# Kernel optimization log

Hardware: AMD Instinct MI355X
Metric: run time of the kernel (lower is better)

Reference implementation:

```python
import jax, jax.numpy as jnp
import numpy as np

B, CIN, COUT, H, W, K = 4, 128, 128, 128, 128, 3
KK = K * K


def setup_inputs() -> dict:
    key = jax.random.key(0)
    ks = jax.random.split(key, 6)
    return {
        "inp": jax.random.normal(ks[0], (B, CIN, H, W), jnp.float32),
        "feat": jax.random.normal(ks[1], (B, CIN, H, W), jnp.float32),
        # small offset-conv weights keep predicted offsets in a realistic few-pixel range
        "w_off": jax.random.normal(ks[2], (3 * KK, CIN, K, K), jnp.float32) * 0.01,
        "b_off": jnp.zeros((3 * KK,), jnp.float32),
        "w_dc": jax.random.normal(ks[3], (COUT, CIN, K, K), jnp.float32) * (1.0 / np.sqrt(CIN * KK)),
        "b_dc": jnp.zeros((COUT,), jnp.float32),
    }


def _conv3x3(x, w, b):
    # stride=1, padding=1, dilation=1, groups=1 (module defaults)
    y = jax.lax.conv_general_dilated(x, w, (1, 1), ((1, 1), (1, 1)),
                                     dimension_numbers=("NCHW", "OIHW", "NCHW"))
    return y + b[None, :, None, None]


def _modulated_deform_conv(x, offset, mask, w, b):
    # DCNv2: offset [B, 2*KK, H, W] interleaved (y, x) per kernel tap, mask [B, KK, H, W]
    b_, c, h, wd = x.shape
    ky = jnp.repeat(jnp.arange(K), K)  # kernel row index per tap, [KK]
    kx = jnp.tile(jnp.arange(K), K)    # kernel col index per tap, [KK]
    off = offset.reshape(b_, KK, 2, h, wd)
    # sampling positions: out_idx - pad + k*dilation + learned offset
    py = off[:, :, 0] + (jnp.arange(h)[None, None, :, None] + ky[None, :, None, None] - 1).astype(offset.dtype)
    px = off[:, :, 1] + (jnp.arange(wd)[None, None, None, :] + kx[None, :, None, None] - 1).astype(offset.dtype)
    y0 = jnp.floor(py)
    x0 = jnp.floor(px)
    ly = py - y0  # bilinear fractions (grad flows to offsets through these)
    lx = px - x0
    y0i = y0.astype(jnp.int32)
    x0i = x0.astype(jnp.int32)
    x_flat = x.reshape(b_, c, h * wd)

    def corner(yi, xi, wgt):
        valid = (yi >= 0) & (yi < h) & (xi >= 0) & (xi < wd)  # zero padding outside
        idx = jnp.clip(yi, 0, h - 1) * wd + jnp.clip(xi, 0, wd - 1)
        g = jnp.take_along_axis(x_flat, idx.reshape(b_, 1, -1), axis=2).reshape(b_, c, KK, h, wd)
        return g * (wgt * valid)[:, None]

    val = (corner(y0i,     x0i,     (1 - ly) * (1 - lx))
         + corner(y0i,     x0i + 1, (1 - ly) * lx)
         + corner(y0i + 1, x0i,     ly * (1 - lx))
         + corner(y0i + 1, x0i + 1, ly * lx))
    val = val * mask[:, None]  # modulation
    out = jnp.einsum("bckhw,ock->bohw", val, w.reshape(w.shape[0], c, KK))
    return out + b[None, :, None, None]


def reference(inp, feat, w_off, b_off, w_dc, b_dc):
    o = _conv3x3(feat, w_off, b_off)
    o1, o2, m = jnp.split(o, 3, axis=1)
    offset = jnp.concatenate([o1, o2], axis=1)
    mask = jax.nn.sigmoid(m)
    return _modulated_deform_conv(inp, offset, mask, w_dc, b_dc)
```

## Files before the change

### kernel.cpp

```cpp
#include <hip/hip_runtime.h>
#include <math.h>

#define B_    4
#define CIN_  128
#define COUT_ 128
#define H_    128
#define W_    128
#define HW_   (H_*W_)
#define KK_   9

typedef __attribute__((ext_vector_type(8))) short short8;
typedef __attribute__((ext_vector_type(4))) float f32x4;
typedef _Float16 h8 __attribute__((ext_vector_type(8)));
typedef float f2v __attribute__((ext_vector_type(2), aligned(4)));

static __device__ __forceinline__ unsigned f2bf(float f) {
    union { float f; unsigned u; } v; v.f = f;
    return (v.u + 0x7fffu + ((v.u >> 16) & 1u)) >> 16;
}
static __device__ __forceinline__ unsigned short f2h(float f) {
    union { _Float16 h; unsigned short u; } v; v.h = (_Float16)f;
    return v.u;
}


__global__ __launch_bounds__(256) void tpose_kernel(
    const float* __restrict__ inp, unsigned short* __restrict__ inpT)
{
    const int by = blockIdx.x;
    const int b = by >> 7, y = by & 127;
    __shared__ unsigned short s_T[128 * 142];

    const float* src = inp + (size_t)b * CIN_ * HW_ + y * W_;
    const int xs = (threadIdx.x & 63) * 2;
    const int c0 = threadIdx.x >> 6;
#pragma unroll 4
    for (int p = 0; p < 32; ++p) {
        int c = c0 + 4 * p;
        f2v d = *(const f2v*)(src + (size_t)c * HW_ + xs);
        s_T[xs * 142 + c]       = f2h(d.x);
        s_T[(xs + 1) * 142 + c] = f2h(d.y);
    }
    __syncthreads();

    unsigned short* dst = inpT + (size_t)by * (W_ * CIN_);
    const int cs = (threadIdx.x & 15) * 8;
    const int x0 = threadIdx.x >> 4;
#pragma unroll
    for (int p = 0; p < 8; ++p) {
        int x = x0 + 16 * p;
        unsigned r[4];
#pragma unroll
        for (int j = 0; j < 4; ++j) {
            unsigned lo = s_T[x * 142 + cs + 2 * j];
            unsigned hi = s_T[x * 142 + cs + 2 * j + 1];
            r[j] = lo | (hi << 16);
        }
        *(int4*)(dst + (size_t)x * CIN_ + cs) = make_int4(r[0], r[1], r[2], r[3]);
    }
}

__global__ __launch_bounds__(256) void wswz_kernel(
    const float* __restrict__ w_dc, unsigned short* __restrict__ w_swz)
{
    int idx = blockIdx.x * 256 + threadIdx.x;
    int q   = idx >> 9;
    int rem = idx & 511;
    int ocb = rem >> 6;
    int l   = rem & 63;
    int cbq = q / 9;
    int k   = q - cbq * 9;
    int cb  = (cbq << 5) + ((l >> 4) << 3);
    int oc  = (ocb << 4) + (l & 15);
    unsigned r[4];
#pragma unroll
    for (int j = 0; j < 4; ++j) {
        float f0 = w_dc[((size_t)(oc * CIN_ + cb + 2 * j    )) * KK_ + k];
        float f1 = w_dc[((size_t)(oc * CIN_ + cb + 2 * j + 1)) * KK_ + k];
        r[j] = (unsigned)f2h(f0) | ((unsigned)f2h(f1) << 16);
    }
    *(int4*)&w_swz[(size_t)idx * 8] = make_int4(r[0], r[1], r[2], r[3]);
}

__global__ __launch_bounds__(256) void woffswz_kernel(
    const float* __restrict__ w_off, unsigned short* __restrict__ woff_swz)
{
    int idx = blockIdx.x * 256 + threadIdx.x;
    int q   = idx >> 7;
    int rem = idx & 127;
    int l   = rem & 63;
    int cbq = q / 9;
    int k   = q - cbq * 9;
    int cb  = (cbq << 5) + ((l >> 4) << 3);
    int oc  = ((rem >> 6) << 4) + (l & 15);
    unsigned r[4];
#pragma unroll
    for (int j = 0; j < 4; ++j) {
        float f0 = 0.f, f1 = 0.f;
        if (oc < 27) {
            f0 = w_off[((size_t)(oc * CIN_ + cb + 2 * j    )) * KK_ + k];
            f1 = w_off[((size_t)(oc * CIN_ + cb + 2 * j + 1)) * KK_ + k];
        }
        r[j] = f2bf(f0) | (f2bf(f1) << 16);
    }
    *(int4*)&woff_swz[(size_t)idx * 8] = make_int4(r[0], r[1], r[2], r[3]);
}

__global__ __launch_bounds__(256, 4) void offset_mfma_kernel(
    const float* __restrict__ feat, const unsigned short* __restrict__ woff_swz,
    const float* __restrict__ b_off, float* __restrict__ offm)
{
    const int tid = threadIdx.x;
    const int bx = blockIdx.x;
    const int lidx = ((bx & 7) << 7) | (bx >> 3);
    const int b  = lidx >> 8;
    const int h  = (lidx & 255) >> 1;
    const int w0 = (lidx & 1) << 6;

    __shared__ unsigned short s_F[3][66][40];

    const int lane = tid & 63;
    const int wave = tid >> 6;
    const int kg = lane >> 4, pn = lane & 15;

    const float* fbase = feat + (size_t)b * CIN_ * HW_;

    f32x4 acc[2];
    acc[0] = (f32x4){0.f, 0.f, 0.f, 0.f};
    acc[1] = (f32x4){0.f, 0.f, 0.f, 0.f};

    for (int cb = 0; cb < 4; ++cb) {
        if (cb) __syncthreads();

#pragma unroll
        for (int r = 0; r < 3; ++r) {
            const int y = h + r - 1;
            const bool yv = (unsigned)y < (unsigned)H_;
            const float* rowp = fbase + (size_t)(cb << 5) * HW_ + y * W_;
#pragma unroll
            for (int j = 0; j < 4; ++j) {
                int item = tid + (j << 8);
                int c = item >> 5;
                int e = item & 31;
                int x0 = w0 - 1 + 2 * e;
                int hx = min(max(x0, 0), W_ - 2);
                float v0 = 0.f, v1 = 0.f;
                if (yv) {
                    f2v p = *(const f2v*)(rowp + (size_t)c * HW_ + hx);
                    v0 = (x0 == hx) ? p.x : ((x0 < hx) ? 0.f : p.y);
                    v1 = (x0 == hx) ? p.y : ((x0 < hx) ? p.x : 0.f);
                }
                s_F[r][2 * e    ][c] = (unsigned short)f2bf(v0);
                s_F[r][2 * e + 1][c] = (unsigned short)f2bf(v1);
            }
            if (tid < 32) {
                int c = tid;
                int x0 = w0 + 63;
                int hx = min(x0, W_ - 2);
                float v0 = 0.f, v1 = 0.f;
                if (yv) {
                    f2v p = *(const f2v*)(rowp + (size_t)c * HW_ + hx);
                    v0 = (x0 == hx) ? p.x : p.y;
                    v1 = (x0 == hx) ? p.y : 0.f;
                }
                s_F[r][64][c] = (unsigned short)f2bf(v0);
                s_F[r][65][c] = (unsigned short)f2bf(v1);
            }
        }
        __syncthreads();

        const int qb2 = cb * 18;
        const short8* wb = (const short8*)woff_swz;
        short8 a0 = wb[(size_t)(qb2    ) * 64 + lane];
        short8 a1 = wb[(size_t)(qb2 + 1) * 64 + lane];
#pragma unroll
        for (int k = 0; k < 9; ++k) {
            const int ky = k / 3, kx = k - 3 * ky;
            short8 bfr = *(const short8*)&s_F[ky][wave * 16 + pn + kx][kg * 8];
            short8 na0, na1;
            if (k < 8) {
                na0 = wb[(size_t)(qb2 + 2 * k + 2) * 64 + lane];
                na1 = wb[(size_t)(qb2 + 2 * k + 3) * 64 + lane];
            }
            acc[0] = __builtin_amdgcn_mfma_f32_16x16x32_bf16(a0, bfr, acc[0], 0, 0, 0);
            acc[1] = __builtin_amdgcn_mfma_f32_16x16x32_bf16(a1, bfr, acc[1], 0, 0, 0);
            if (k < 8) { a0 = na0; a1 = na1; }
        }
    }

    const int row0 = (lane >> 4) << 2;
    const int col  = lane & 15;
    const int pw   = w0 + wave * 16 + col;
#pragma unroll
    for (int mt = 0; mt < 2; ++mt) {
#pragma unroll
        for (int i = 0; i < 4; ++i) {
            int oc = mt * 16 + row0 + i;
            if (oc < 27) {
                float v = acc[mt][i] + b_off[oc];
                if (oc >= 18) v = 1.f / (1.f + __expf(-v));
                offm[((size_t)(b * 27 + oc)) * HW_ + h * W_ + pw] = v;
            }
        }
    }
}

__global__ __launch_bounds__(256, 4) void dcn_mfma_kernel(
    const unsigned short* __restrict__ inpT, const float* __restrict__ offm,
    const unsigned short* __restrict__ w_swz, const float* __restrict__ b_dc,
    float* __restrict__ out)
{
    const int tid = threadIdx.x;
    const int bx = blockIdx.x;
    const int lidx = ((bx & 7) << 7) | (bx >> 3);
    const int b   = lidx >> 8;
    const int h   = (lidx & 255) >> 1;
    const int pw0 = (lidx & 1) << 6;

    __shared__ int2   s_midx[576];
    __shared__ float4 s_mwgt[576];
    __shared__ unsigned short s_V[2][64][40];

    for (int i = tid; i < 576; i += 256) {
        int k = i >> 6, p = i & 63;
        int ky = k / 3, kx = k - ky * 3;
        int pw = pw0 + p;
        const float* ob = offm + (size_t)b * 27 * HW_ + h * W_ + pw;
        float offy = ob[(2 * k    ) * HW_];
        float offx = ob[(2 * k + 1) * HW_];
        float mask = ob[(18 + k   ) * HW_];
        float py = offy + (float)(h  + ky - 1);
        float px_ = offx + (float)(pw + kx - 1);
        float y0f = floorf(py), x0f = floorf(px_);
        float ly = py - y0f, lx = px_ - x0f;
        int y0 = (int)y0f, x0 = (int)x0f;
        int y1 = y0 + 1;
        int hx = min(max(x0, 0), W_ - 2);
        float wlo = 0.f, whi = 0.f;
        if (x0 == hx)          { wlo = 1.f - lx; whi = lx; }
        else if (x0 == hx - 1) { wlo = lx; }
        else if (x0 == hx + 1) { whi = 1.f - lx; }
        float wt_top = ((unsigned)y0 < (unsigned)H_) ? (1.f - ly) * mask : 0.f;
        float wt_bot = ((unsigned)y1 < (unsigned)H_) ? ly * mask : 0.f;
        int cy0 = min(max(y0, 0), H_ - 1), cy1 = min(max(y1, 0), H_ - 1);
        s_midx[i] = make_int2(cy0 * W_ + hx, cy1 * W_ + hx);
        s_mwgt[i] = make_float4(wt_top * wlo, wt_top * whi,
                                wt_bot * wlo, wt_bot * whi);
    }

    const int lane = tid & 63;
    const int wave = tid >> 6;
    const int kg = lane >> 4, pn = lane & 15;
    const int px = tid >> 2;
    const int cs = tid & 3;

    const char* inpTb = (const char*)(inpT + (size_t)b * CIN_ * HW_);

    f32x4 acc[2][4];
#pragma unroll
    for (int mt = 0; mt < 2; ++mt)
#pragma unroll
        for (int nt = 0; nt < 4; ++nt) acc[mt][nt] = (f32x4){0.f, 0.f, 0.f, 0.f};

    h8 pf0, pf1, pf2, pf3;

    auto issue = [&](int qq) {
        int cbq = qq / 9;
        int k   = qq - cbq * 9;
        int2 id = s_midx[(k << 6) + px];
        int coff = (cbq << 6) + (cs << 4);
        const char* g0 = inpTb + ((size_t)(unsigned)id.x << 8) + coff;
        const char* g1 = inpTb + ((size_t)(unsigned)id.y << 8) + coff;
        pf0 = *(const h8*)(g0);
        pf1 = *(const h8*)(g0 + 256);
        pf2 = *(const h8*)(g1);
        pf3 = *(const h8*)(g1 + 256);
    };

    __syncthreads();
    issue(0);

    for (int q = 0; q < 36; ++q) {
        int k = q - (q / 9) * 9;

        float4 wt = s_mwgt[(k << 6) + px];
        h8 v = pf0 * (_Float16)wt.x;
        v += pf1 * (_Float16)wt.y;
        v += pf2 * (_Float16)wt.z;
        v += pf3 * (_Float16)wt.w;

        const h8* wp = (const h8*)w_swz + (size_t)(q * 8 + wave * 2) * 64 + lane;
        h8 af0 = wp[0];
        h8 af1 = wp[64];

        *(h8*)&s_V[q & 1][px][cs << 3] = v;

        int qn = (q + 1 < 36) ? q + 1 : 35;
        issue(qn);

        __syncthreads();

#pragma unroll
        for (int nt = 0; nt < 4; ++nt) {
            h8 bfr = *(const h8*)&s_V[q & 1][nt * 16 + pn][kg * 8];
            acc[0][nt] = __builtin_amdgcn_mfma_f32_16x16x32_f16(af0, bfr, acc[0][nt], 0, 0, 0);
            acc[1][nt] = __builtin_amdgcn_mfma_f32_16x16x32_f16(af1, bfr, acc[1][nt], 0, 0, 0);
        }
    }

    const int row0 = (lane >> 4) << 2;
    const int col  = lane & 15;
#pragma unroll
    for (int mt = 0; mt < 2; ++mt) {
#pragma unroll
        for (int nt = 0; nt < 4; ++nt) {
            int pw = pw0 + nt * 16 + col;
#pragma unroll
            for (int i = 0; i < 4; ++i) {
                int oc = wave * 32 + mt * 16 + row0 + i;
                out[((size_t)(b * COUT_ + oc)) * HW_ + h * W_ + pw] =
                    acc[mt][nt][i] + b_dc[oc];
            }
        }
    }
}

extern "C" void kernel_launch(void* const* d_in, const int* in_sizes, int n_in,
                              void* d_out, int out_size, void* d_ws, size_t ws_size,
                              hipStream_t stream)
{
    const float* inp   = (const float*)d_in[0];
    const float* feat  = (const float*)d_in[1];
    const float* w_off = (const float*)d_in[2];
    const float* b_off = (const float*)d_in[3];
    const float* w_dc  = (const float*)d_in[4];
    const float* b_dc  = (const float*)d_in[5];
    float* out  = (float*)d_out;
    float* offm = (float*)d_ws;
    unsigned short* w_swz    = (unsigned short*)((char*)d_ws + 7077888);
    unsigned short* woff_swz = (unsigned short*)((char*)d_ws + 7077888 + 294912);
    unsigned short* inpT     = (unsigned short*)((char*)d_ws + 7446528);

    tpose_kernel<<<dim3(512), dim3(256), 0, stream>>>(inp, inpT);
    woffswz_kernel<<<dim3(18), dim3(256), 0, stream>>>(w_off, woff_swz);
    wswz_kernel<<<dim3(72), dim3(256), 0, stream>>>(w_dc, w_swz);
    offset_mfma_kernel<<<dim3(1024), dim3(256), 0, stream>>>(feat, woff_swz, b_off, offm);
    dcn_mfma_kernel<<<dim3(1024), dim3(256), 0, stream>>>(inpT, offm, w_swz, b_dc, out);
}
```

Before: 186.7 us.

## Fuse offset conv into deformable conv kernel and merge prep kernels

The three preprocessing kernels (input transpose, weight swizzles) are merged into one launch dispatched by block index. The offset/mask convolution is fused into the deformable-conv kernel, so offsets stay in shared memory instead of passing through a global workspace buffer. Shared memory is aliased between the feature tile and the sampled-value buffer. The per-thread pixel/channel mapping for the gather also changes from px=tid>>2 to px=tid&63, which alters the gather's memory access pattern. This removes two launches and the offset-map round trip, at the cost of a longer single kernel with more shared memory and possibly fewer resident blocks.

```diff
diff --git a/kernel.cpp b/kernel.cpp
--- a/kernel.cpp
+++ b/kernel.cpp
@@ -24,91 +24,89 @@
 }
 
 
-__global__ __launch_bounds__(256) void tpose_kernel(
-    const float* __restrict__ inp, unsigned short* __restrict__ inpT)
+__global__ __launch_bounds__(256) void prep_kernel(
+    const float* __restrict__ inp, const float* __restrict__ w_dc,
+    const float* __restrict__ w_off, unsigned short* __restrict__ inpT,
+    unsigned short* __restrict__ w_swz, unsigned short* __restrict__ woff_swz)
 {
-    const int by = blockIdx.x;
-    const int b = by >> 7, y = by & 127;
+    const int bx = blockIdx.x;
+    const int tid = threadIdx.x;
     __shared__ unsigned short s_T[128 * 142];
 
-    const float* src = inp + (size_t)b * CIN_ * HW_ + y * W_;
-    const int xs = (threadIdx.x & 63) * 2;
-    const int c0 = threadIdx.x >> 6;
+    if (bx < 512) {
+        const int b = bx >> 7, y = bx & 127;
+        const float* src = inp + (size_t)b * CIN_ * HW_ + y * W_;
+        const int xs = (tid & 63) * 2;
+        const int c0 = tid >> 6;
 #pragma unroll 4
-    for (int p = 0; p < 32; ++p) {
-        int c = c0 + 4 * p;
-        f2v d = *(const f2v*)(src + (size_t)c * HW_ + xs);
-        s_T[xs * 142 + c]       = f2h(d.x);
-        s_T[(xs + 1) * 142 + c] = f2h(d.y);
-    }
-    __syncthreads();
-
-    unsigned short* dst = inpT + (size_t)by * (W_ * CIN_);
-    const int cs = (threadIdx.x & 15) * 8;
-    const int x0 = threadIdx.x >> 4;
-#pragma unroll
-    for (int p = 0; p < 8; ++p) {
-        int x = x0 + 16 * p;
+        for (int p = 0; p < 32; ++p) {
+            int c = c0 + 4 * p;
+            f2v d = *(const f2v*)(src + (size_t)c * HW_ + xs);
+            s_T[xs * 142 + c]       = f2h(d.x);
+            s_T[(xs + 1) * 142 + c] = f2h(d.y);
+        }
+        __syncthreads();
+        unsigned short* dst = inpT + (size_t)bx * (W_ * CIN_);
+        const int cs = (tid & 15) * 8;
+        const int x0 = tid >> 4;
+#pragma unroll
+        for (int p = 0; p < 8; ++p) {
+            int x = x0 + 16 * p;
+            unsigned r[4];
+#pragma unroll
+            for (int j = 0; j < 4; ++j) {
+                unsigned lo = s_T[x * 142 + cs + 2 * j];
+                unsigned hi = s_T[x * 142 + cs + 2 * j + 1];
+                r[j] = lo | (hi << 16);
+            }
+            *(int4*)(dst + (size_t)x * CIN_ + cs) = make_int4(r[0], r[1], r[2], r[3]);
+        }
+    } else if (bx < 584) {
+        int idx = (bx - 512) * 256 + tid;
+        int q   = idx >> 9;
+        int rem = idx & 511;
+        int ocb = rem >> 6;
+        int l   = rem & 63;
+        int cbq = q / 9;
+        int k   = q - cbq * 9;
+        int cb  = (cbq << 5) + ((l >> 4) << 3);
+        int oc  = (ocb << 4) + (l & 15);
         unsigned r[4];
 #pragma unroll
         for (int j = 0; j < 4; ++j) {
-            unsigned lo = s_T[x * 142 + cs + 2 * j];
-            unsigned hi = s_T[x * 142 + cs + 2 * j + 1];
-            r[j] = lo | (hi << 16);
-        }
-        *(int4*)(dst + (size_t)x * CIN_ + cs) = make_int4(r[0], r[1], r[2], r[3]);
-    }
-}
-
-__global__ __launch_bounds__(256) void wswz_kernel(
-    const float* __restrict__ w_dc, unsigned short* __restrict__ w_swz)
-{
-    int idx = blockIdx.x * 256 + threadIdx.x;
-    int q   = idx >> 9;
-    int rem = idx & 511;
-    int ocb = rem >> 6;
-    int l   = rem & 63;
-    int cbq = q / 9;
-    int k   = q - cbq * 9;
-    int cb  = (cbq << 5) + ((l >> 4) << 3);
-    int oc  = (ocb << 4) + (l & 15);
-    unsigned r[4];
-#pragma unroll
-    for (int j = 0; j < 4; ++j) {
-        float f0 = w_dc[((size_t)(oc * CIN_ + cb + 2 * j    )) * KK_ + k];
-        float f1 = w_dc[((size_t)(oc * CIN_ + cb + 2 * j + 1)) * KK_ + k];
-        r[j] = (unsigned)f2h(f0) | ((unsigned)f2h(f1) << 16);
-    }
-    *(int4*)&w_swz[(size_t)idx * 8] = make_int4(r[0], r[1], r[2], r[3]);
-}
-
-__global__ __launch_bounds__(256) void woffswz_kernel(
-    const float* __restrict__ w_off, unsigned short* __restrict__ woff_swz)
-{
-    int idx = blockIdx.x * 256 + threadIdx.x;
-    int q   = idx >> 7;
-    int rem = idx & 127;
-    int l   = rem & 63;
-    int cbq = q / 9;
-    int k   = q - cbq * 9;
-    int cb  = (cbq << 5) + ((l >> 4) << 3);
-    int oc  = ((rem >> 6) << 4) + (l & 15);
-    unsigned r[4];
-#pragma unroll
-    for (int j = 0; j < 4; ++j) {
-        float f0 = 0.f, f1 = 0.f;
-        if (oc < 27) {
-            f0 = w_off[((size_t)(oc * CIN_ + cb + 2 * j    )) * KK_ + k];
-            f1 = w_off[((size_t)(oc * CIN_ + cb + 2 * j + 1)) * KK_ + k];
-        }
-        r[j] = f2bf(f0) | (f2bf(f1) << 16);
-    }
-    *(int4*)&woff_swz[(size_t)idx * 8] = make_int4(r[0], r[1], r[2], r[3]);
-}
-
-__global__ __launch_bounds__(256, 4) void offset_mfma_kernel(
-    const float* __restrict__ feat, const unsigned short* __restrict__ woff_swz,
-    const float* __restrict__ b_off, float* __restrict__ offm)
+            float f0 = w_dc[((size_t)(oc * CIN_ + cb + 2 * j    )) * KK_ + k];
+            float f1 = w_dc[((size_t)(oc * CIN_ + cb + 2 * j + 1)) * KK_ + k];
+            r[j] = (unsigned)f2h(f0) | ((unsigned)f2h(f1) << 16);
+        }
+        *(int4*)&w_swz[(size_t)idx * 8] = make_int4(r[0], r[1], r[2], r[3]);
+    } else {
+        int idx = (bx - 584) * 256 + tid;
+        int q   = idx >> 7;
+        int rem = idx & 127;
+        int l   = rem & 63;
+        int cbq = q / 9;
+        int k   = q - cbq * 9;
+        int cb  = (cbq << 5) + ((l >> 4) << 3);
+        int oc  = ((rem >> 6) << 4) + (l & 15);
+        unsigned r[4];
+#pragma unroll
+        for (int j = 0; j < 4; ++j) {
+            float f0 = 0.f, f1 = 0.f;
+            if (oc < 27) {
+                f0 = w_off[((size_t)(oc * CIN_ + cb + 2 * j    )) * KK_ + k];
+                f1 = w_off[((size_t)(oc * CIN_ + cb + 2 * j + 1)) * KK_ + k];
+            }
+            r[j] = f2bf(f0) | (f2bf(f1) << 16);
+        }
+        *(int4*)&woff_swz[(size_t)idx * 8] = make_int4(r[0], r[1], r[2], r[3]);
+    }
+}
+
+__global__ __launch_bounds__(256, 4) void fused_kernel(
+    const float* __restrict__ feat, const unsigned short* __restrict__ inpT,
+    const unsigned short* __restrict__ woff_swz, const unsigned short* __restrict__ w_swz,
+    const float* __restrict__ b_off, const float* __restrict__ b_dc,
+    float* __restrict__ out)
 {
     const int tid = threadIdx.x;
     const int bx = blockIdx.x;
@@ -117,119 +115,108 @@
     const int h  = (lidx & 255) >> 1;
     const int w0 = (lidx & 1) << 6;
 
-    __shared__ unsigned short s_F[3][66][40];
+    __shared__ __align__(16) char smem[36736];
+    unsigned short (*s_F)[66][40] = (unsigned short (*)[66][40])smem;
+    unsigned short *s_Vb          = (unsigned short*)smem;
+    float  (*offv)[65]            = (float (*)[65])(smem + 15872);
+    int2   *s_midx                = (int2  *)(smem + 15872 + 7040);
+    float4 *s_mwgt                = (float4*)(smem + 15872 + 7040 + 4608);
 
     const int lane = tid & 63;
     const int wave = tid >> 6;
     const int kg = lane >> 4, pn = lane & 15;
 
-    const float* fbase = feat + (size_t)b * CIN_ * HW_;
-
-    f32x4 acc[2];
-    acc[0] = (f32x4){0.f, 0.f, 0.f, 0.f};
-    acc[1] = (f32x4){0.f, 0.f, 0.f, 0.f};
-
-    for (int cb = 0; cb < 4; ++cb) {
-        if (cb) __syncthreads();
-
-#pragma unroll
-        for (int r = 0; r < 3; ++r) {
-            const int y = h + r - 1;
-            const bool yv = (unsigned)y < (unsigned)H_;
-            const float* rowp = fbase + (size_t)(cb << 5) * HW_ + y * W_;
-#pragma unroll
-            for (int j = 0; j < 4; ++j) {
-                int item = tid + (j << 8);
-                int c = item >> 5;
-                int e = item & 31;
-                int x0 = w0 - 1 + 2 * e;
-                int hx = min(max(x0, 0), W_ - 2);
-                float v0 = 0.f, v1 = 0.f;
-                if (yv) {
-                    f2v p = *(const f2v*)(rowp + (size_t)c * HW_ + hx);
-                    v0 = (x0 == hx) ? p.x : ((x0 < hx) ? 0.f : p.y);
-                    v1 = (x0 == hx) ? p.y : ((x0 < hx) ? p.x : 0.f);
+    {
+        const float* fbase = feat + (size_t)b * CIN_ * HW_;
+        f32x4 acc[2];
+        acc[0] = (f32x4){0.f, 0.f, 0.f, 0.f};
+        acc[1] = (f32x4){0.f, 0.f, 0.f, 0.f};
+
+        for (int cb = 0; cb < 4; ++cb) {
+            if (cb) __syncthreads();
+
+#pragma unroll
+            for (int r = 0; r < 3; ++r) {
+                const int y = h + r - 1;
+                const bool yv = (unsigned)y < (unsigned)H_;
+                const float* rowp = fbase + (size_t)(cb << 5) * HW_ + y * W_;
+#pragma unroll
+                for (int j = 0; j < 4; ++j) {
+                    int item = tid + (j << 8);
+                    int c = item >> 5;
+                    int e = item & 31;
+                    int x0 = w0 - 1 + 2 * e;
+                    int hx = min(max(x0, 0), W_ - 2);
+                    float v0 = 0.f, v1 = 0.f;
+                    if (yv) {
+                        f2v p = *(const f2v*)(rowp + (size_t)c * HW_ + hx);
+                        v0 = (x0 == hx) ? p.x : ((x0 < hx) ? 0.f : p.y);
+                        v1 = (x0 == hx) ? p.y : ((x0 < hx) ? p.x : 0.f);
+                    }
+                    s_F[r][2 * e    ][c] = (unsigned short)f2bf(v0);
+                    s_F[r][2 * e + 1][c] = (unsigned short)f2bf(v1);
                 }
-                s_F[r][2 * e    ][c] = (unsigned short)f2bf(v0);
-                s_F[r][2 * e + 1][c] = (unsigned short)f2bf(v1);
-            }
-            if (tid < 32) {
-                int c = tid;
-                int x0 = w0 + 63;
-                int hx = min(x0, W_ - 2);
-                float v0 = 0.f, v1 = 0.f;
-                if (yv) {
-                    f2v p = *(const f2v*)(rowp + (size_t)c * HW_ + hx);
-                    v0 = (x0 == hx) ? p.x : p.y;
-                    v1 = (x0 == hx) ? p.y : 0.f;
+                if (tid < 32) {
+                    int c = tid;
+                    int x0 = w0 + 63;
+                    int hx = min(x0, W_ - 2);
+                    float v0 = 0.f, v1 = 0.f;
+                    if (yv) {
+                        f2v p = *(const f2v*)(rowp + (size_t)c * HW_ + hx);
+                        v0 = (x0 == hx) ? p.x : p.y;
+                        v1 = (x0 == hx) ? p.y : 0.f;
+                    }
+                    s_F[r][64][c] = (unsigned short)f2bf(v0);
+                    s_F[r][65][c] = (unsigned short)f2bf(v1);
                 }
-                s_F[r][64][c] = (unsigned short)f2bf(v0);
-                s_F[r][65][c] = (unsigned short)f2bf(v1);
-            }
-        }
-        __syncthreads();
-
-        const int qb2 = cb * 18;
-        const short8* wb = (const short8*)woff_swz;
-        short8 a0 = wb[(size_t)(qb2    ) * 64 + lane];
-        short8 a1 = wb[(size_t)(qb2 + 1) * 64 + lane];
-#pragma unroll
-        for (int k = 0; k < 9; ++k) {
-            const int ky = k / 3, kx = k - 3 * ky;
-            short8 bfr = *(const short8*)&s_F[ky][wave * 16 + pn + kx][kg * 8];
-            short8 na0, na1;
-            if (k < 8) {
-                na0 = wb[(size_t)(qb2 + 2 * k + 2) * 64 + lane];
-                na1 = wb[(size_t)(qb2 + 2 * k + 3) * 64 + lane];
-            }
-            acc[0] = __builtin_amdgcn_mfma_f32_16x16x32_bf16(a0, bfr, acc[0], 0, 0, 0);
-            acc[1] = __builtin_amdgcn_mfma_f32_16x16x32_bf16(a1, bfr, acc[1], 0, 0, 0);
-            if (k < 8) { a0 = na0; a1 = na1; }
-        }
-    }
-
-    const int row0 = (lane >> 4) << 2;
-    const int col  = lane & 15;
-    const int pw   = w0 + wave * 16 + col;
-#pragma unroll
-    for (int mt = 0; mt < 2; ++mt) {
-#pragma unroll
-        for (int i = 0; i < 4; ++i) {
-            int oc = mt * 16 + row0 + i;
-            if (oc < 27) {
-                float v = acc[mt][i] + b_off[oc];
-                if (oc >= 18) v = 1.f / (1.f + __expf(-v));
-                offm[((size_t)(b * 27 + oc)) * HW_ + h * W_ + pw] = v;
-            }
-        }
-    }
-}
-
-__global__ __launch_bounds__(256, 4) void dcn_mfma_kernel(
-    const unsigned short* __restrict__ inpT, const float* __restrict__ offm,
-    const unsigned short* __restrict__ w_swz, const float* __restrict__ b_dc,
-    float* __restrict__ out)
-{
-    const int tid = threadIdx.x;
-    const int bx = blockIdx.x;
-    const int lidx = ((bx & 7) << 7) | (bx >> 3);
-    const int b   = lidx >> 8;
-    const int h   = (lidx & 255) >> 1;
-    const int pw0 = (lidx & 1) << 6;
-
-    __shared__ int2   s_midx[576];
-    __shared__ float4 s_mwgt[576];
-    __shared__ unsigned short s_V[2][64][40];
+            }
+            __syncthreads();
+
+            const int qb2 = cb * 18;
+            const short8* wb = (const short8*)woff_swz;
+            short8 a0 = wb[(size_t)(qb2    ) * 64 + lane];
+            short8 a1 = wb[(size_t)(qb2 + 1) * 64 + lane];
+#pragma unroll
+            for (int k = 0; k < 9; ++k) {
+                const int ky = k / 3, kx = k - 3 * ky;
+                short8 bfr = *(const short8*)&s_F[ky][wave * 16 + pn + kx][kg * 8];
+                short8 na0, na1;
+                if (k < 8) {
+                    na0 = wb[(size_t)(qb2 + 2 * k + 2) * 64 + lane];
+                    na1 = wb[(size_t)(qb2 + 2 * k + 3) * 64 + lane];
+                }
+                acc[0] = __builtin_amdgcn_mfma_f32_16x16x32_bf16(a0, bfr, acc[0], 0, 0, 0);
+                acc[1] = __builtin_amdgcn_mfma_f32_16x16x32_bf16(a1, bfr, acc[1], 0, 0, 0);
+                if (k < 8) { a0 = na0; a1 = na1; }
+            }
+        }
+
+        const int row0 = (lane >> 4) << 2;
+        const int col  = lane & 15;
+        const int pwl  = wave * 16 + col;
+#pragma unroll
+        for (int mt = 0; mt < 2; ++mt) {
+#pragma unroll
+            for (int i = 0; i < 4; ++i) {
+                int oc = mt * 16 + row0 + i;
+                if (oc < 27) {
+                    float v = acc[mt][i] + b_off[oc];
+                    if (oc >= 18) v = 1.f / (1.f + __expf(-v));
+                    offv[oc][pwl] = v;
+                }
+            }
+        }
+    }
+    __syncthreads();
 
     for (int i = tid; i < 576; i += 256) {
         int k = i >> 6, p = i & 63;
         int ky = k / 3, kx = k - ky * 3;
-        int pw = pw0 + p;
-        const float* ob = offm + (size_t)b * 27 * HW_ + h * W_ + pw;
-        float offy = ob[(2 * k    ) * HW_];
-        float offx = ob[(2 * k + 1) * HW_];
-        float mask = ob[(18 + k   ) * HW_];
-        float py = offy + (float)(h  + ky - 1);
+        int pw = w0 + p;
+        float offy = offv[2 * k    ][p];
+        float offx = offv[2 * k + 1][p];
+        float mask = offv[18 + k   ][p];
+        float py  = offy + (float)(h  + ky - 1);
         float px_ = offx + (float)(pw + kx - 1);
         float y0f = floorf(py), x0f = floorf(px_);
         float ly = py - y0f, lx = px_ - x0f;
@@ -247,20 +234,17 @@
         s_mwgt[i] = make_float4(wt_top * wlo, wt_top * whi,
                                 wt_bot * wlo, wt_bot * whi);
     }
-
-    const int lane = tid & 63;
-    const int wave = tid >> 6;
-    const int kg = lane >> 4, pn = lane & 15;
-    const int px = tid >> 2;
-    const int cs = tid & 3;
-
+    __syncthreads();
+
+    const int px = tid & 63;
+    const int cs = tid >> 6;
     const char* inpTb = (const char*)(inpT + (size_t)b * CIN_ * HW_);
 
-    f32x4 acc[2][4];
+    f32x4 acc2[2][4];
 #pragma unroll
     for (int mt = 0; mt < 2; ++mt)
 #pragma unroll
-        for (int nt = 0; nt < 4; ++nt) acc[mt][nt] = (f32x4){0.f, 0.f, 0.f, 0.f};
+        for (int nt = 0; nt < 4; ++nt) acc2[mt][nt] = (f32x4){0.f, 0.f, 0.f, 0.f};
 
     h8 pf0, pf1, pf2, pf3;
 
@@ -277,7 +261,6 @@
         pf3 = *(const h8*)(g1 + 256);
     };
 
-    __syncthreads();
     issue(0);
 
     for (int q = 0; q < 36; ++q) {
@@ -293,7 +276,7 @@
         h8 af0 = wp[0];
         h8 af1 = wp[64];
 
-        *(h8*)&s_V[q & 1][px][cs << 3] = v;
+        *(h8*)&s_Vb[(size_t)(q & 1) * (64 * 40) + px * 40 + (cs << 3)] = v;
 
         int qn = (q + 1 < 36) ? q + 1 : 35;
         issue(qn);
@@ -302,9 +285,9 @@
 
 #pragma unroll
         for (int nt = 0; nt < 4; ++nt) {
-            h8 bfr = *(const h8*)&s_V[q & 1][nt * 16 + pn][kg * 8];
-            acc[0][nt] = __builtin_amdgcn_mfma_f32_16x16x32_f16(af0, bfr, acc[0][nt], 0, 0, 0);
-            acc[1][nt] = __builtin_amdgcn_mfma_f32_16x16x32_f16(af1, bfr, acc[1][nt], 0, 0, 0);
+            h8 bfr = *(const h8*)&s_Vb[(size_t)(q & 1) * (64 * 40) + (nt * 16 + pn) * 40 + kg * 8];
+            acc2[0][nt] = __builtin_amdgcn_mfma_f32_16x16x32_f16(af0, bfr, acc2[0][nt], 0, 0, 0);
+            acc2[1][nt] = __builtin_amdgcn_mfma_f32_16x16x32_f16(af1, bfr, acc2[1][nt], 0, 0, 0);
         }
     }
 
@@ -314,12 +297,12 @@
     for (int mt = 0; mt < 2; ++mt) {
 #pragma unroll
         for (int nt = 0; nt < 4; ++nt) {
-            int pw = pw0 + nt * 16 + col;
+            int pw = w0 + nt * 16 + col;
 #pragma unroll
             for (int i = 0; i < 4; ++i) {
                 int oc = wave * 32 + mt * 16 + row0 + i;
                 out[((size_t)(b * COUT_ + oc)) * HW_ + h * W_ + pw] =
-                    acc[mt][nt][i] + b_dc[oc];
+                    acc2[mt][nt][i] + b_dc[oc];
             }
         }
     }
@@ -336,14 +319,10 @@
     const float* w_dc  = (const float*)d_in[4];
     const float* b_dc  = (const float*)d_in[5];
     float* out  = (float*)d_out;
-    float* offm = (float*)d_ws;
-    unsigned short* w_swz    = (unsigned short*)((char*)d_ws + 7077888);
-    unsigned short* woff_swz = (unsigned short*)((char*)d_ws + 7077888 + 294912);
-    unsigned short* inpT     = (unsigned short*)((char*)d_ws + 7446528);
-
-    tpose_kernel<<<dim3(512), dim3(256), 0, stream>>>(inp, inpT);
-    woffswz_kernel<<<dim3(18), dim3(256), 0, stream>>>(w_off, woff_swz);
-    wswz_kernel<<<dim3(72), dim3(256), 0, stream>>>(w_dc, w_swz);
-    offset_mfma_kernel<<<dim3(1024), dim3(256), 0, stream>>>(feat, woff_swz, b_off, offm);
-    dcn_mfma_kernel<<<dim3(1024), dim3(256), 0, stream>>>(inpT, offm, w_swz, b_dc, out);
-}
+    unsigned short* w_swz    = (unsigned short*)d_ws;
+    unsigned short* woff_swz = (unsigned short*)((char*)d_ws + 294912);
+    unsigned short* inpT     = (unsigned short*)((char*)d_ws + 368640);
+
+    prep_kernel<<<dim3(602), dim3(256), 0, stream>>>(inp, w_dc, w_off, inpT, w_swz, woff_swz);
+    fused_kernel<<<dim3(1024), dim3(256), 0, stream>>>(feat, inpT, woff_swz, w_swz, b_off, b_dc, out);
+}
```

Result: slower. 208.6 us (+11.7%).
